# Optimization experiments

Measured on AMD Instinct MI355X. Metric: run time of the kernel, lower is better.

Reference implementation:

```python
import jax, jax.numpy as jnp
import numpy as np

NHEAD = 8
LN_EPS = 1e-5


def _l2norm(x, eps=1e-6):
    # matches torch.nn.functional.normalize(p=2, eps=eps)
    n = jnp.linalg.norm(x, axis=-1, keepdims=True)
    return x / jnp.maximum(n, eps)


def setup_inputs() -> dict:
    key = jax.random.key(0)
    ks = jax.random.split(key, 10)
    Q, B, D = 100, 16, 256
    T, Dc = 8192, 768
    s = lambda d: 1.0 / np.sqrt(d)
    return {
        "tgt": jax.random.normal(ks[0], (Q, B, D), jnp.float32),
        "text_classification": jax.random.normal(ks[1], (B, T, Dc), jnp.float32),
        "query_pos": jax.random.normal(ks[2], (Q, B, D), jnp.float32),
        "out_of_vocab_logits": jax.random.normal(ks[3], (B, Q, T), jnp.float32),
        "Wq": jax.random.normal(ks[4], (D, D), jnp.float32) * s(D),
        "bq": jnp.zeros((D,), jnp.float32),
        "Wk": jax.random.normal(ks[5], (D, Dc), jnp.float32) * s(Dc),
        "bk": jnp.zeros((D,), jnp.float32),
        "Wv": jax.random.normal(ks[6], (D, Dc), jnp.float32) * s(Dc),
        "bv": jnp.zeros((D,), jnp.float32),
        "Wo": jax.random.normal(ks[7], (D, D), jnp.float32) * s(D),
        "bo": jnp.zeros((D,), jnp.float32),
        "ln_g": jnp.ones((D,), jnp.float32),
        "ln_b": jnp.zeros((D,), jnp.float32),
        "log_scale": jnp.asarray(np.log(1.0 / 0.07), jnp.float32),
    }


def reference(tgt, text_classification, query_pos, out_of_vocab_logits,
              Wq, bq, Wk, bk, Wv, bv, Wo, bo, ln_g, ln_b, log_scale):
    Qn, B, D = tgt.shape
    T = text_classification.shape[1]
    H = NHEAD
    hd = D // H

    # forward_post: q = tgt + query_pos ; k = v = text_classification
    q_in = tgt + query_pos                                   # [Q, B, D]
    q = jnp.einsum('qbd,ed->qbe', q_in, Wq) + bq             # [Q, B, D]
    k = jnp.einsum('btc,ec->bte', text_classification, Wk) + bk  # [B, T, D]
    v = jnp.einsum('btc,ec->bte', text_classification, Wv) + bv  # [B, T, D]

    # split heads -> [B, H, L, hd]
    q = q.transpose(1, 0, 2).reshape(B, Qn, H, hd).transpose(0, 2, 1, 3)
    k = k.reshape(B, T, H, hd).transpose(0, 2, 1, 3)
    v = v.reshape(B, T, H, hd).transpose(0, 2, 1, 3)

    q = _l2norm(q)
    k = _l2norm(k)
    scale = jnp.minimum(jnp.exp(log_scale), 100.0)
    logits = jnp.einsum('bhqd,bhkd->bhqk', q, k) * scale     # [B, H, Q, T]

    # per-head ensemble with out-of-vocab logits
    alpha = jnp.linspace(0.0, 1.0, H, dtype=logits.dtype).reshape(1, H, 1, 1)
    logits = logits * (1.0 - alpha) + out_of_vocab_logits[:, None] * alpha

    attn = jax.nn.softmax(logits, axis=-1)
    out = jnp.einsum('bhqk,bhkd->bhqd', attn, v)             # [B, H, Q, hd]
    out = out.transpose(0, 2, 1, 3).reshape(B, Qn, D).transpose(1, 0, 2)  # [Q, B, D]
    out = jnp.einsum('qbd,ed->qbe', out, Wo) + bo

    # residual + LayerNorm (post-norm)
    x = tgt + out
    mu = x.mean(axis=-1, keepdims=True)
    var = x.var(axis=-1, keepdims=True)
    x = (x - mu) * jax.lax.rsqrt(var + LN_EPS) * ln_g + ln_b
    return x
```

## Files before the change

kernel.cpp:

```cpp
#include <hip/hip_runtime.h>
#include <hip/hip_bf16.h>

#define QN 100
#define QP 112
#define BB 16
#define DD 256
#define TT 8192
#define DC 768
#define HH 8
#define HD 32
#define SL16 16
#define NPART 32

typedef short bf16x4 __attribute__((ext_vector_type(4)));
typedef short bf16x8 __attribute__((ext_vector_type(8)));
typedef float f32x4 __attribute__((ext_vector_type(4)));
typedef _Float16 half4 __attribute__((ext_vector_type(4)));

__global__ __launch_bounds__(256) void qproj_kernel(
    const float* __restrict__ tgt, const float* __restrict__ qpos,
    const float* __restrict__ Wq, const float* __restrict__ bq,
    ushort* __restrict__ Qhi, ushort* __restrict__ Qlo) {
  int bid = blockIdx.x;
  int q = bid >> 4, b = bid & 15;
  int e = threadIdx.x;
  int h = e >> 5, d = e & 31;
  size_t widx = ((size_t)(b * HH + h) * QP + q) * HD + d;
  if (q >= QN) { Qhi[widx] = 0; Qlo[widx] = 0; return; }
  __shared__ float arow[DD];
  size_t off = ((size_t)q * BB + b) * DD + e;
  arow[e] = tgt[off] + qpos[off];
  __syncthreads();
  const float4* w4 = (const float4*)(Wq + (size_t)e * DD);
  const float4* a4 = (const float4*)arow;
  float acc = bq[e];
#pragma unroll 8
  for (int i = 0; i < DD / 4; ++i) {
    float4 wv = w4[i], av = a4[i];
    acc += wv.x * av.x + wv.y * av.y + wv.z * av.z + wv.w * av.w;
  }
  float ss = acc * acc;
#pragma unroll
  for (int o = 16; o; o >>= 1) ss += __shfl_xor(ss, o, 64);
  float qn = acc * (1.0f / fmaxf(sqrtf(ss), 1e-6f));
  uint u = __float_as_uint(qn);
  float hif = __uint_as_float(u & 0xffff0000u);
  Qhi[widx] = (ushort)(u >> 16);
  Qlo[widx] = (ushort)(__float_as_uint(qn - hif) >> 16);
}

#define KV_CONVERT(RAF)                                                       \
  {                                                                           \
    const float* raf = (const float*)(RAF);                                   \
    _Pragma("unroll") for (int g = 0; g < 4; ++g) {                           \
      uint hiw[4], low[4];                                                    \
      _Pragma("unroll") for (int p2 = 0; p2 < 4; ++p2) {                      \
        float f0 = raf[8 * g + 2 * p2], f1 = raf[8 * g + 2 * p2 + 1];         \
        uint b0 = __float_as_uint(f0), b1 = __float_as_uint(f1);              \
        float h0 = __uint_as_float(b0 & 0xffff0000u);                         \
        float h1 = __uint_as_float(b1 & 0xffff0000u);                         \
        hiw[p2] = (b0 >> 16) | (b1 & 0xffff0000u);                            \
        low[p2] = (__float_as_uint(f0 - h0) >> 16) |                          \
                  (__float_as_uint(f1 - h1) & 0xffff0000u);                   \
      }                                                                       \
      *(uint4*)&dhi[g][r][0] = make_uint4(hiw[0], hiw[1], hiw[2], hiw[3]);    \
      *(uint4*)&dlo[g][r][0] = make_uint4(low[0], low[1], low[2], low[3]);    \
    }                                                                         \
  }

#define KV_MFMA()                                                             \
  {                                                                           \
    bf16x8 bhf[4], blf[4];                                                    \
    _Pragma("unroll") for (int ni = 0; ni < 4; ++ni) {                        \
      int row = wn * 64 + ni * 16 + fr;                                       \
      bhf[ni] = *(const bf16x8*)&Bhi[kg][row][0];                             \
      blf[ni] = *(const bf16x8*)&Blo[kg][row][0];                             \
    }                                                                         \
    _Pragma("unroll") for (int mi = 0; mi < 4; ++mi) {                        \
      int row = wm * 64 + mi * 16 + fr;                                       \
      bf16x8 ah = *(const bf16x8*)&Ahi[kg][row][0];                           \
      bf16x8 al = *(const bf16x8*)&Alo[kg][row][0];                           \
      _Pragma("unroll") for (int ni = 0; ni < 4; ++ni) {                      \
        acc[mi][ni] = __builtin_amdgcn_mfma_f32_16x16x32_bf16(                \
            ah, bhf[ni], acc[mi][ni], 0, 0, 0);                               \
        acc[mi][ni] = __builtin_amdgcn_mfma_f32_16x16x32_bf16(                \
            ah, blf[ni], acc[mi][ni], 0, 0, 0);                               \
        acc[mi][ni] = __builtin_amdgcn_mfma_f32_16x16x32_bf16(                \
            al, bhf[ni], acc[mi][ni], 0, 0, 0);                               \
      }                                                                       \
    }                                                                         \
  }

__global__ __launch_bounds__(256) void kv_gemm_kernel(
    const float* __restrict__ text,
    const float* __restrict__ Wk, const float* __restrict__ bk,
    const float* __restrict__ Wv, const float* __restrict__ bv,
    float* __restrict__ Kout, float* __restrict__ Vout) {
  __shared__ short Ahi[4][129][8];
  __shared__ short Alo[4][129][8];
  __shared__ short Bhi[4][129][8];
  __shared__ short Blo[4][129][8];

  int bid = blockIdx.x;
  int w = (bid & 7) * 512 + (bid >> 3);
  int mt = w >> 2, nt = w & 3;
  int m0 = mt * 128, n0 = nt * 128;
  int tid = threadIdx.x;

  const float* Wbase = (n0 < 256) ? Wk : Wv;
  const float* bias_vec = (n0 < 256) ? bk : bv;
  float* dst = (n0 < 256) ? Kout : Vout;
  int ncol0 = n0 & 255;

  int r = tid & 127;
  bool isA = tid < 128;
  const float* src = isA ? (text + (size_t)(m0 + r) * DC)
                         : (Wbase + (size_t)(ncol0 + r) * DC);
  short (*dhi)[129][8] = isA ? Ahi : Bhi;
  short (*dlo)[129][8] = isA ? Alo : Blo;

  int lane = tid & 63, wid = tid >> 6;
  int wm = wid >> 1, wn = wid & 1;
  int kg = lane >> 4, fr = lane & 15;

  f32x4 acc[4][4];
#pragma unroll
  for (int i = 0; i < 4; ++i)
#pragma unroll
    for (int j = 0; j < 4; ++j) acc[i][j] = (f32x4){0.f, 0.f, 0.f, 0.f};

  float4 raA[8], raB[8];
#pragma unroll
  for (int c = 0; c < 8; ++c) raA[c] = *(const float4*)(src + c * 4);

  for (int ks = 0; ks < 24; ks += 2) {
    {
      const float* s2 = src + (ks + 1) * 32;
#pragma unroll
      for (int c = 0; c < 8; ++c) raB[c] = *(const float4*)(s2 + c * 4);
    }
    KV_CONVERT(raA);
    __syncthreads();
    KV_MFMA();
    __syncthreads();
    if (ks + 2 < 24) {
      const float* s3 = src + (ks + 2) * 32;
#pragma unroll
      for (int c = 0; c < 8; ++c) raA[c] = *(const float4*)(s3 + c * 4);
    }
    KV_CONVERT(raB);
    __syncthreads();
    KV_MFMA();
    __syncthreads();
  }

#pragma unroll
  for (int ni = 0; ni < 4; ++ni) {
    int col = n0 + wn * 64 + ni * 16 + fr;
    int e = col & 255;
    int h = e >> 5, d = e & 31;
    float bias = bias_vec[e];
#pragma unroll
    for (int mi = 0; mi < 4; ++mi) {
      f32x4 c = acc[mi][ni];
      int mbase = m0 + wm * 64 + mi * 16 + kg * 4;
#pragma unroll
      for (int j = 0; j < 4; ++j) {
        int m = mbase + j;
        int b = m >> 13, t = m & 8191;
        dst[(((size_t)(b * HH + h)) * TT + t) * HD + d] = c[j] + bias;
      }
    }
  }
}

__global__ __launch_bounds__(256) void prep_kernel(float* __restrict__ Kbuf,
                                                   float* __restrict__ Vbuf) {
  __shared__ float vl[32][257];
  int c = blockIdx.x;
  int tid = threadIdx.x;
  float* Kc = Kbuf + (size_t)c * 8192;
  float* Vc = Vbuf + (size_t)c * 8192;

  float kr[32];
#pragma unroll
  for (int i = 0; i < 8; ++i)
    *(float4*)&kr[i * 4] = *(const float4*)(Kc + (size_t)tid * 32 + i * 4);
#pragma unroll
  for (int i = 0; i < 8; ++i) {
    float4 v = *(const float4*)(Vc + (size_t)tid * 32 + i * 4);
    vl[i * 4 + 0][tid] = v.x;
    vl[i * 4 + 1][tid] = v.y;
    vl[i * 4 + 2][tid] = v.z;
    vl[i * 4 + 3][tid] = v.w;
  }
  __syncthreads();

  float ss = 0.f;
#pragma unroll
  for (int i = 0; i < 32; ++i) ss += kr[i] * kr[i];
  float rk = 1.0f / fmaxf(sqrtf(ss), 1e-6f);
  ushort* Kh = (ushort*)Kc;
  uint hiw[16], low[16];
#pragma unroll
  for (int p = 0; p < 16; ++p) {
    float f0 = kr[2 * p] * rk, f1 = kr[2 * p + 1] * rk;
    uint b0 = __float_as_uint(f0), b1 = __float_as_uint(f1);
    float h0 = __uint_as_float(b0 & 0xffff0000u);
    float h1 = __uint_as_float(b1 & 0xffff0000u);
    hiw[p] = (b0 >> 16) | (b1 & 0xffff0000u);
    low[p] = (__float_as_uint(f0 - h0) >> 16) |
             (__float_as_uint(f1 - h1) & 0xffff0000u);
  }
#pragma unroll
  for (int i = 0; i < 4; ++i) {
    *(uint4*)(Kh + (size_t)tid * 32 + i * 8) =
        make_uint4(hiw[4 * i], hiw[4 * i + 1], hiw[4 * i + 2], hiw[4 * i + 3]);
    *(uint4*)(Kh + 8192 + (size_t)tid * 32 + i * 8) =
        make_uint4(low[4 * i], low[4 * i + 1], low[4 * i + 2], low[4 * i + 3]);
  }

  int d = tid & 31, c8 = tid >> 5;
  float vv[32];
#pragma unroll
  for (int t = 0; t < 32; ++t) vv[t] = vl[d][c8 * 32 + t];
  ushort* Vh = (ushort*)Vc;
#pragma unroll
  for (int p = 0; p < 16; ++p) {
    float f0 = vv[2 * p], f1 = vv[2 * p + 1];
    uint b0 = __float_as_uint(f0), b1 = __float_as_uint(f1);
    float h0 = __uint_as_float(b0 & 0xffff0000u);
    float h1 = __uint_as_float(b1 & 0xffff0000u);
    hiw[p] = (b0 >> 16) | (b1 & 0xffff0000u);
    low[p] = (__float_as_uint(f0 - h0) >> 16) |
             (__float_as_uint(f1 - h1) & 0xffff0000u);
  }
#pragma unroll
  for (int i = 0; i < 4; ++i) {
    *(uint4*)(Vh + (size_t)d * 256 + c8 * 32 + i * 8) =
        make_uint4(hiw[4 * i], hiw[4 * i + 1], hiw[4 * i + 2], hiw[4 * i + 3]);
    *(uint4*)(Vh + 8192 + (size_t)d * 256 + c8 * 32 + i * 8) =
        make_uint4(low[4 * i], low[4 * i + 1], low[4 * i + 2], low[4 * i + 3]);
  }
}

__global__ __launch_bounds__(256) void oovt_kernel(
    const float* __restrict__ oov, ushort* __restrict__ oovT) {
  __shared__ ushort tile[64][116];
  int bidx = blockIdx.x;
  int b = bidx >> 7, tc = (bidx & 127) * 64;
  int tid = threadIdx.x;
#pragma unroll
  for (int rr = 0; rr < 25; ++rr) {
    int idx = rr * 256 + tid;
    int q = idx >> 6, tt = idx & 63;
    float v = oov[((size_t)b * QN + q) * TT + tc + tt];
    tile[tt][q] = __builtin_bit_cast(ushort, (_Float16)v);
  }
#pragma unroll
  for (int rr = 0; rr < 3; ++rr) {
    int idx = rr * 256 + tid;
    tile[idx & 63][100 + (idx >> 6)] = 0;
  }
  __syncthreads();
#pragma unroll
  for (int rr = 0; rr < 7; ++rr) {
    int idx = rr * 256 + tid;
    int tt = idx / 28, jj = idx - tt * 28;
    int q0 = jj * 4;
    *(uint2*)(oovT + (((size_t)b * TT + tc + tt) << 7) + q0) =
        *(const uint2*)&tile[tt][q0];
  }
}

__global__ __launch_bounds__(128, 3) void attn_kernel(
    const ushort* __restrict__ Qhi, const ushort* __restrict__ Qlo,
    const ushort* __restrict__ Kpl, const ushort* __restrict__ Vpl,
    const ushort* __restrict__ oovT, const float* __restrict__ log_scale,
    float* __restrict__ pacc, float* __restrict__ pl) {
  __shared__ short Pbuf[2][QP][36];
  int bid = blockIdx.x;
  int sl = bid & 15, bh = bid >> 4;
  int b = bh >> 3, h = bh & 7;
  int tid = threadIdx.x, lane = tid & 63, w = tid >> 6;
  int fr = lane & 15, kg = lane >> 4;

  float scale = fminf(__expf(log_scale[0]), 100.0f);
  float alpha = (float)h * (1.0f / 7.0f);
  float cs = scale * (1.0f - alpha);

  f32x4 oacc[7][2];
#pragma unroll
  for (int qt = 0; qt < 7; ++qt)
#pragma unroll
    for (int dt = 0; dt < 2; ++dt) oacc[qt][dt] = (f32x4){0.f, 0.f, 0.f, 0.f};
  float lsum[7][4];
#pragma unroll
  for (int qt = 0; qt < 7; ++qt)
#pragma unroll
    for (int j = 0; j < 4; ++j) lsum[qt][j] = 0.f;

  short* Ph = &Pbuf[w][0][0];
  const size_t qbase = (size_t)bh * QP * HD;

  for (int s = 0; s < 8; ++s) {
    int t0 = sl * 512 + s * 64 + w * 32;
    int c = bh * 32 + (t0 >> 8);
    int ttb = t0 & 255;
    const ushort* Kc = Kpl + (size_t)c * 16384;
    const ushort* Vc = Vpl + (size_t)c * 16384;

    bf16x8 kh[2], kl[2];
#pragma unroll
    for (int tt = 0; tt < 2; ++tt) {
      int off = (ttb + tt * 16 + fr) * HD + kg * 8;
      kh[tt] = *(const bf16x8*)(Kc + off);
      kl[tt] = *(const bf16x8*)(Kc + 8192 + off);
    }
    const ushort* ovb = oovT + (((size_t)b * TT + t0) << 7);

#pragma unroll
    for (int qt = 0; qt < 7; ++qt) {
      size_t qa = qbase + (size_t)(qt * 16 + fr) * HD + kg * 8;
      bf16x8 qh = *(const bf16x8*)(Qhi + qa);
      bf16x8 ql = *(const bf16x8*)(Qlo + qa);
#pragma unroll
      for (int tt = 0; tt < 2; ++tt) {
        f32x4 sacc = (f32x4){0.f, 0.f, 0.f, 0.f};
        sacc = __builtin_amdgcn_mfma_f32_16x16x32_bf16(qh, kh[tt], sacc, 0, 0, 0);
        sacc = __builtin_amdgcn_mfma_f32_16x16x32_bf16(ql, kh[tt], sacc, 0, 0, 0);
        sacc = __builtin_amdgcn_mfma_f32_16x16x32_bf16(qh, kl[tt], sacc, 0, 0, 0);
        half4 hv = *(const half4*)(ovb + (size_t)(tt * 16 + fr) * 128 + qt * 16 + kg * 4);
#pragma unroll
        for (int j = 0; j < 4; ++j) {
          float S = __expf(sacc[j] * cs + (float)hv[j] * alpha);
          uint u = __float_as_uint(S) & 0xffff0000u;
          lsum[qt][j] += __uint_as_float(u);
          Ph[(qt * 16 + kg * 4 + j) * 36 + tt * 16 + fr] = (short)(u >> 16);
        }
      }
    }

    bf16x8 vh[2], vlo[2];
#pragma unroll
    for (int dt = 0; dt < 2; ++dt) {
      int off = (dt * 16 + fr) * 256 + ttb + kg * 8;
      vh[dt] = *(const bf16x8*)(Vc + off);
      vlo[dt] = *(const bf16x8*)(Vc + 8192 + off);
    }
#pragma unroll
    for (int qt = 0; qt < 7; ++qt) {
      int qrow = qt * 16 + fr;
      bf16x4 p0 = *(const bf16x4*)&Ph[qrow * 36 + kg * 8];
      bf16x4 p1 = *(const bf16x4*)&Ph[qrow * 36 + kg * 8 + 4];
      bf16x8 pv8 = __builtin_shufflevector(p0, p1, 0, 1, 2, 3, 4, 5, 6, 7);
#pragma unroll
      for (int dt = 0; dt < 2; ++dt) {
        oacc[qt][dt] = __builtin_amdgcn_mfma_f32_16x16x32_bf16(pv8, vh[dt], oacc[qt][dt], 0, 0, 0);
        oacc[qt][dt] = __builtin_amdgcn_mfma_f32_16x16x32_bf16(pv8, vlo[dt], oacc[qt][dt], 0, 0, 0);
      }
    }
  }

#pragma unroll
  for (int qt = 0; qt < 7; ++qt)
#pragma unroll
    for (int j = 0; j < 4; ++j) {
      float v = lsum[qt][j];
      v += __shfl_xor(v, 1, 64);
      v += __shfl_xor(v, 2, 64);
      v += __shfl_xor(v, 4, 64);
      v += __shfl_xor(v, 8, 64);
      lsum[qt][j] = v;
    }
  int ps = bh * NPART + sl * 2 + w;
  size_t pb = (size_t)ps * QN;
#pragma unroll
  for (int qt = 0; qt < 7; ++qt)
#pragma unroll
    for (int dt = 0; dt < 2; ++dt)
#pragma unroll
      for (int j = 0; j < 4; ++j) {
        int q = qt * 16 + kg * 4 + j;
        if (q < QN) pacc[(pb + q) * HD + dt * 16 + fr] = oacc[qt][dt][j];
      }
  if (fr == 0) {
#pragma unroll
    for (int qt = 0; qt < 7; ++qt)
#pragma unroll
      for (int j = 0; j < 4; ++j) {
        int q = qt * 16 + kg * 4 + j;
        if (q < QN) pl[pb + q] = lsum[qt][j];
      }
  }
}

__global__ __launch_bounds__(256) void out_kernel(
    const float* __restrict__ part_acc, const float* __restrict__ part_l,
    const float* __restrict__ Wo, const float* __restrict__ bo,
    const float* __restrict__ tgt, const float* __restrict__ ln_g,
    const float* __restrict__ ln_b, float* __restrict__ out) {
  int bid = blockIdx.x;
  int q = bid >> 4, b = bid & 15;
  int e = threadIdx.x;
  int h = e >> 5, d = e & 31;
  __shared__ float row[DD];
  __shared__ float r1[4], r2[4];

  size_t base = ((size_t)(b * HH + h)) * NPART * QN + q;
  float a = 0.0f, lt = 0.0f;
#pragma unroll 8
  for (int s = 0; s < NPART; ++s) {
    a += part_acc[(base + (size_t)s * QN) * HD + d];
    lt += part_l[base + (size_t)s * QN];
  }
  row[e] = a / lt;
  __syncthreads();

  const float4* w4 = (const float4*)(Wo + (size_t)e * DD);
  const float4* r4 = (const float4*)row;
  float o = bo[e];
#pragma unroll 8
  for (int i = 0; i < DD / 4; ++i) {
    float4 wv = w4[i], rv = r4[i];
    o += wv.x * rv.x + wv.y * rv.y + wv.z * rv.z + wv.w * rv.w;
  }
  float x = tgt[((size_t)q * BB + b) * DD + e] + o;

  float s1 = x, s2 = x * x;
#pragma unroll
  for (int off = 32; off; off >>= 1) {
    s1 += __shfl_xor(s1, off, 64);
    s2 += __shfl_xor(s2, off, 64);
  }
  int wid = e >> 6, lane = e & 63;
  if (lane == 0) { r1[wid] = s1; r2[wid] = s2; }
  __syncthreads();
  float T1 = r1[0] + r1[1] + r1[2] + r1[3];
  float T2 = r2[0] + r2[1] + r2[2] + r2[3];
  float mu = T1 * (1.0f / DD);
  float var = T2 * (1.0f / DD) - mu * mu;
  out[((size_t)q * BB + b) * DD + e] =
      (x - mu) * rsqrtf(var + 1e-5f) * ln_g[e] + ln_b[e];
}

extern "C" void kernel_launch(void* const* d_in, const int* in_sizes, int n_in,
                              void* d_out, int out_size, void* d_ws, size_t ws_size,
                              hipStream_t stream) {
  (void)in_sizes; (void)n_in; (void)out_size; (void)ws_size;
  const float* tgt  = (const float*)d_in[0];
  const float* text = (const float*)d_in[1];
  const float* qpos = (const float*)d_in[2];
  const float* oov  = (const float*)d_in[3];
  const float* Wq = (const float*)d_in[4];
  const float* bq = (const float*)d_in[5];
  const float* Wk = (const float*)d_in[6];
  const float* bk = (const float*)d_in[7];
  const float* Wv = (const float*)d_in[8];
  const float* bv = (const float*)d_in[9];
  const float* Wo = (const float*)d_in[10];
  const float* bo = (const float*)d_in[11];
  const float* ln_g = (const float*)d_in[12];
  const float* ln_b = (const float*)d_in[13];
  const float* log_scale = (const float*)d_in[14];
  float* out = (float*)d_out;

  char* wsb = (char*)d_ws;
  ushort* Qhi = (ushort*)wsb;
  ushort* Qlo = Qhi + (size_t)BB * HH * QP * HD;
  float* Kbuf = (float*)(wsb + 2u * 917504u);
  float* Vbuf = Kbuf + (size_t)BB * HH * TT * HD;
  ushort* oovT = (ushort*)(Vbuf + (size_t)BB * HH * TT * HD);
  float* pacc = (float*)((char*)oovT + (size_t)BB * TT * 128 * 2);
  float* pl   = pacc + (size_t)BB * HH * NPART * QN * HD;

  hipLaunchKernelGGL(qproj_kernel, dim3(QP * BB), dim3(DD), 0, stream,
                     tgt, qpos, Wq, bq, Qhi, Qlo);
  hipLaunchKernelGGL(kv_gemm_kernel, dim3(4096), dim3(256), 0, stream,
                     text, Wk, bk, Wv, bv, Kbuf, Vbuf);
  hipLaunchKernelGGL(prep_kernel, dim3(4096), dim3(256), 0, stream,
                     Kbuf, Vbuf);
  hipLaunchKernelGGL(oovt_kernel, dim3(BB * 128), dim3(256), 0, stream,
                     oov, oovT);
  hipLaunchKernelGGL(attn_kernel, dim3(BB * HH * SL16), dim3(128), 0, stream,
                     Qhi, Qlo, (const ushort*)Kbuf, (const ushort*)Vbuf,
                     oovT, log_scale, pacc, pl);
  hipLaunchKernelGGL(out_kernel, dim3(QN * BB), dim3(DD), 0, stream,
                     pacc, pl, Wo, bo, tgt, ln_g, ln_b, out);
}
```

Measured before the change: 1.385 ms.

## Prefetch next K tile and V early in attention loop, use exp2

Software-pipelines the attention loop. The next iteration's K fragments are loaded during the PV MFMA phase, and the current V fragments are issued at the start of the iteration, so global load latency overlaps compute. The exponent uses exp2f with log2e folded into the scale constants. The occupancy hint of 3 blocks per CU is dropped from launch bounds, which may raise register use and lower occupancy. The last iteration also performs one redundant wrapped K prefetch.

```diff
diff --git a/kernel.cpp b/kernel.cpp
--- a/kernel.cpp
+++ b/kernel.cpp
@@ -273,7 +273,7 @@
   }
 }
 
-__global__ __launch_bounds__(128, 3) void attn_kernel(
+__global__ __launch_bounds__(128) void attn_kernel(
     const ushort* __restrict__ Qhi, const ushort* __restrict__ Qlo,
     const ushort* __restrict__ Kpl, const ushort* __restrict__ Vpl,
     const ushort* __restrict__ oovT, const float* __restrict__ log_scale,
@@ -285,9 +285,11 @@
   int tid = threadIdx.x, lane = tid & 63, w = tid >> 6;
   int fr = lane & 15, kg = lane >> 4;
 
+  const float LOG2E = 1.4426950408889634f;
   float scale = fminf(__expf(log_scale[0]), 100.0f);
   float alpha = (float)h * (1.0f / 7.0f);
-  float cs = scale * (1.0f - alpha);
+  float cs2 = scale * (1.0f - alpha) * LOG2E;
+  float al2 = alpha * LOG2E;
 
   f32x4 oacc[7][2];
 #pragma unroll
@@ -302,20 +304,33 @@
 
   short* Ph = &Pbuf[w][0][0];
   const size_t qbase = (size_t)bh * QP * HD;
+
+  bf16x8 khA[2], klA[2];
+  {
+    int t0 = sl * 512 + w * 32;
+    int c = bh * 32 + (t0 >> 8);
+    int ttb = t0 & 255;
+    const ushort* Kc = Kpl + (size_t)c * 16384;
+#pragma unroll
+    for (int tt = 0; tt < 2; ++tt) {
+      int off = (ttb + tt * 16 + fr) * HD + kg * 8;
+      khA[tt] = *(const bf16x8*)(Kc + off);
+      klA[tt] = *(const bf16x8*)(Kc + 8192 + off);
+    }
+  }
 
   for (int s = 0; s < 8; ++s) {
     int t0 = sl * 512 + s * 64 + w * 32;
     int c = bh * 32 + (t0 >> 8);
     int ttb = t0 & 255;
-    const ushort* Kc = Kpl + (size_t)c * 16384;
     const ushort* Vc = Vpl + (size_t)c * 16384;
 
-    bf16x8 kh[2], kl[2];
-#pragma unroll
-    for (int tt = 0; tt < 2; ++tt) {
-      int off = (ttb + tt * 16 + fr) * HD + kg * 8;
-      kh[tt] = *(const bf16x8*)(Kc + off);
-      kl[tt] = *(const bf16x8*)(Kc + 8192 + off);
+    bf16x8 vh[2], vlo[2];
+#pragma unroll
+    for (int dt = 0; dt < 2; ++dt) {
+      int off = (dt * 16 + fr) * 256 + ttb + kg * 8;
+      vh[dt] = *(const bf16x8*)(Vc + off);
+      vlo[dt] = *(const bf16x8*)(Vc + 8192 + off);
     }
     const ushort* ovb = oovT + (((size_t)b * TT + t0) << 7);
 
@@ -327,13 +342,13 @@
 #pragma unroll
       for (int tt = 0; tt < 2; ++tt) {
         f32x4 sacc = (f32x4){0.f, 0.f, 0.f, 0.f};
-        sacc = __builtin_amdgcn_mfma_f32_16x16x32_bf16(qh, kh[tt], sacc, 0, 0, 0);
-        sacc = __builtin_amdgcn_mfma_f32_16x16x32_bf16(ql, kh[tt], sacc, 0, 0, 0);
-        sacc = __builtin_amdgcn_mfma_f32_16x16x32_bf16(qh, kl[tt], sacc, 0, 0, 0);
+        sacc = __builtin_amdgcn_mfma_f32_16x16x32_bf16(qh, khA[tt], sacc, 0, 0, 0);
+        sacc = __builtin_amdgcn_mfma_f32_16x16x32_bf16(ql, khA[tt], sacc, 0, 0, 0);
+        sacc = __builtin_amdgcn_mfma_f32_16x16x32_bf16(qh, klA[tt], sacc, 0, 0, 0);
         half4 hv = *(const half4*)(ovb + (size_t)(tt * 16 + fr) * 128 + qt * 16 + kg * 4);
 #pragma unroll
         for (int j = 0; j < 4; ++j) {
-          float S = __expf(sacc[j] * cs + (float)hv[j] * alpha);
+          float S = exp2f(sacc[j] * cs2 + (float)hv[j] * al2);
           uint u = __float_as_uint(S) & 0xffff0000u;
           lsum[qt][j] += __uint_as_float(u);
           Ph[(qt * 16 + kg * 4 + j) * 36 + tt * 16 + fr] = (short)(u >> 16);
@@ -341,13 +356,21 @@
       }
     }
 
-    bf16x8 vh[2], vlo[2];
-#pragma unroll
-    for (int dt = 0; dt < 2; ++dt) {
-      int off = (dt * 16 + fr) * 256 + ttb + kg * 8;
-      vh[dt] = *(const bf16x8*)(Vc + off);
-      vlo[dt] = *(const bf16x8*)(Vc + 8192 + off);
-    }
+    bf16x8 khB[2], klB[2];
+    {
+      int sn = (s + 1) & 7;
+      int t0n = sl * 512 + sn * 64 + w * 32;
+      int cn = bh * 32 + (t0n >> 8);
+      int ttbn = t0n & 255;
+      const ushort* Kn = Kpl + (size_t)cn * 16384;
+#pragma unroll
+      for (int tt = 0; tt < 2; ++tt) {
+        int off = (ttbn + tt * 16 + fr) * HD + kg * 8;
+        khB[tt] = *(const bf16x8*)(Kn + off);
+        klB[tt] = *(const bf16x8*)(Kn + 8192 + off);
+      }
+    }
+
 #pragma unroll
     for (int qt = 0; qt < 7; ++qt) {
       int qrow = qt * 16 + fr;
@@ -360,6 +383,9 @@
         oacc[qt][dt] = __builtin_amdgcn_mfma_f32_16x16x32_bf16(pv8, vlo[dt], oacc[qt][dt], 0, 0, 0);
       }
     }
+
+    khA[0] = khB[0]; khA[1] = khB[1];
+    klA[0] = klB[0]; klA[1] = klB[1];
   }
 
 #pragma unroll
```

Result: faster. 1.333 ms (-3.7%).
